# Performance work log

Hardware: AMD Instinct MI355X
Metric: run time of the kernel (lower is better)

Reference implementation:

```python
import jax, jax.numpy as jnp
import numpy as np

N, E, C, O, H, W, K = 32, 512, 64, 128, 64, 64, 3


def setup_inputs() -> dict:
    key = jax.random.key(0)
    k1, k2, k3, k4, k5, k6 = jax.random.split(key, 6)
    scale_w = 1.0 / np.sqrt(E)
    return {
        "embedding": jax.random.normal(k1, (N, E), dtype=jnp.float32),
        "images": jax.random.normal(k2, (N, C, H, W), dtype=jnp.float32),
        "w_weight": jax.random.uniform(k3, (O * C * K * K, E), dtype=jnp.float32, minval=-scale_w, maxval=scale_w),
        "w_bias": jax.random.uniform(k4, (O * C * K * K,), dtype=jnp.float32, minval=-scale_w, maxval=scale_w),
        "b_weight": jax.random.uniform(k5, (O, E), dtype=jnp.float32, minval=-scale_w, maxval=scale_w),
        "b_bias": jax.random.uniform(k6, (O,), dtype=jnp.float32, minval=-scale_w, maxval=scale_w),
    }


def reference(embedding, images, w_weight, w_bias, b_weight, b_bias):
    n, c, h, w = images.shape
    o = b_bias.shape[0]
    # per-sample generated filters and biases
    c1_w = embedding @ w_weight.T + w_bias          # [N, O*C*K*K]
    c1_b = embedding @ b_weight.T + b_bias          # [N, O]
    filt = c1_w.reshape(n, o, c, K, K)              # matches torch view(O, C*K*K)
    # im2col equivalent: pad then gather 3x3 shifted views -> [N,C,K,K,H,W]
    xp = jnp.pad(images, ((0, 0), (0, 0), (1, 1), (1, 1)))
    patches = jnp.stack(
        [xp[:, :, i:i + h, j:j + w] for i in range(K) for j in range(K)], axis=2
    ).reshape(n, c, K, K, h, w)
    out = jnp.einsum('nocij,ncijhw->nohw', filt, patches)
    return out + c1_b[:, :, None, None]
```

## Files before the change

### kernel.cpp

```cpp
#include <hip/hip_runtime.h>
#include <hip/hip_bf16.h>

#define N_  32
#define E_  512
#define C_  64
#define O_  128
#define H_  64
#define W_  64
#define CK9 576
#define M_  (O_*CK9)
#define IMGP_ROWB 9216

typedef __bf16 bf16x8 __attribute__((ext_vector_type(8)));
typedef __bf16 bf16x4 __attribute__((ext_vector_type(4)));
typedef float  f32x4  __attribute__((ext_vector_type(4)));

__device__ __forceinline__ void gload_lds16(const void* g, void* l) {
    typedef __attribute__((address_space(1))) const void gvoid;
    typedef __attribute__((address_space(3))) void lvoid;
    __builtin_amdgcn_global_load_lds((gvoid*)g, (lvoid*)l, 16, 0, 0);
}

__global__ __launch_bounds__(256) void img_pack(
    const float* __restrict__ img, __bf16* __restrict__ imgp)
{
    __shared__ __align__(16) __bf16 ldsT[64 * 72];

    int tid = threadIdx.x;
    int blk = blockIdx.x;
    int n = blk / 66, hh = blk - n * 66;
    char* dst = (char*)imgp + ((size_t)n * 66 + hh) * IMGP_ROWB;

    bf16x8 zero = {(__bf16)0.f, (__bf16)0.f, (__bf16)0.f, (__bf16)0.f,
                   (__bf16)0.f, (__bf16)0.f, (__bf16)0.f, (__bf16)0.f};

    if (hh == 0 || hh == 65) {
#pragma unroll
        for (int j = 0; j < 3; j++) {
            int u = j * 256 + tid;
            if (u < 576) *reinterpret_cast<bf16x8*>(dst + u * 16) = zero;
        }
        return;
    }

    int h = hh - 1;
    const float* srcn = img + (size_t)n * (C_ * H_ * W_) + h * 64;
#pragma unroll
    for (int i = 0; i < 4; i++) {
        int idx = i * 256 + tid;
        int c = idx >> 4, wq = (idx & 15) * 4;
        f32x4 v = *reinterpret_cast<const f32x4*>(srcn + (size_t)c * 4096 + wq);
#pragma unroll
        for (int j = 0; j < 4; j++)
            ldsT[(wq + j) * 72 + c] = (__bf16)v[j];
    }
    __syncthreads();

#pragma unroll
    for (int j = 0; j < 3; j++) {
        int u = j * 256 + tid;
        if (u < 576) {
            int col = u >> 3, s = u & 7;
            bf16x8 val = zero;
            if (col >= 1 && col <= 64) {
                int b = s ^ (col & 7);
                val = *reinterpret_cast<const bf16x8*>(&ldsT[(col - 1) * 72 + b * 8]);
            }
            *reinterpret_cast<bf16x8*>(dst + u * 16) = val;
        }
    }
}

__global__ __launch_bounds__(256) void gen_filters(
    const float* __restrict__ emb, const float* __restrict__ w_weight,
    const float* __restrict__ w_bias, __bf16* __restrict__ filt)
{
    __shared__ __align__(16) __bf16 embS[32 * 520];
    __shared__ __align__(16) __bf16 wS[128 * 40];

    int tid  = threadIdx.x;
    int wave = tid >> 6, lane = tid & 63;
    int quad = lane >> 4, l16 = lane & 15;
    int m0 = blockIdx.x * 128;

#pragma unroll
    for (int i = 0; i < 16; i++) {
        int idx = (i * 256 + tid) * 4;
        int n = idx >> 9, e = idx & 511;
        f32x4 v = *reinterpret_cast<const f32x4*>(emb + n * 512 + e);
        bf16x4 b;
        b[0] = (__bf16)v[0]; b[1] = (__bf16)v[1]; b[2] = (__bf16)v[2]; b[3] = (__bf16)v[3];
        *reinterpret_cast<bf16x4*>(&embS[n * 520 + e]) = b;
    }

    f32x4 acc[2][2];
#pragma unroll
    for (int mi = 0; mi < 2; mi++)
#pragma unroll
        for (int ni = 0; ni < 2; ni++)
            acc[mi][ni] = (f32x4){0.f, 0.f, 0.f, 0.f};

    int sub = tid & 7, rbase = tid >> 3;

    for (int kk = 0; kk < 16; kk++) {
        int k0 = kk * 32;
        __syncthreads();
#pragma unroll
        for (int q = 0; q < 4; q++) {
            int row = rbase + q * 32;
            f32x4 v = *reinterpret_cast<const f32x4*>(
                w_weight + (size_t)(m0 + row) * 512 + k0 + sub * 4);
            bf16x4 b;
            b[0] = (__bf16)v[0]; b[1] = (__bf16)v[1]; b[2] = (__bf16)v[2]; b[3] = (__bf16)v[3];
            *reinterpret_cast<bf16x4*>(&wS[row * 40 + sub * 4]) = b;
        }
        __syncthreads();

        bf16x8 a0 = *reinterpret_cast<const bf16x8*>(&wS[(wave * 32 + l16) * 40 + quad * 8]);
        bf16x8 a1 = *reinterpret_cast<const bf16x8*>(&wS[(wave * 32 + 16 + l16) * 40 + quad * 8]);
        bf16x8 b0 = *reinterpret_cast<const bf16x8*>(&embS[l16 * 520 + k0 + quad * 8]);
        bf16x8 b1 = *reinterpret_cast<const bf16x8*>(&embS[(16 + l16) * 520 + k0 + quad * 8]);
        acc[0][0] = __builtin_amdgcn_mfma_f32_16x16x32_bf16(a0, b0, acc[0][0], 0, 0, 0);
        acc[0][1] = __builtin_amdgcn_mfma_f32_16x16x32_bf16(a0, b1, acc[0][1], 0, 0, 0);
        acc[1][0] = __builtin_amdgcn_mfma_f32_16x16x32_bf16(a1, b0, acc[1][0], 0, 0, 0);
        acc[1][1] = __builtin_amdgcn_mfma_f32_16x16x32_bf16(a1, b1, acc[1][1], 0, 0, 0);
    }

#pragma unroll
    for (int mi = 0; mi < 2; mi++) {
#pragma unroll
        for (int r = 0; r < 4; r++) {
            int m = m0 + wave * 32 + mi * 16 + quad * 4 + r;
            int o = m / 576;
            int rem = m - o * 576;
            int c = rem / 9;
            int t = rem - c * 9;
            int kp = t * 64 + c;
            size_t base = ((size_t)(kp >> 3) << 10) + ((size_t)o << 3) + (kp & 7);
            float bias = w_bias[m];
#pragma unroll
            for (int ni = 0; ni < 2; ni++) {
                int n = ni * 16 + l16;
                filt[(size_t)n * M_ + base] = (__bf16)(acc[mi][ni][r] + bias);
            }
        }
    }
}

__global__ __launch_bounds__(256) void gen_bias(
    const float* __restrict__ emb, const float* __restrict__ b_weight,
    const float* __restrict__ b_bias, float* __restrict__ c1b)
{
    int wid  = (blockIdx.x * 256 + threadIdx.x) >> 6;
    int lane = threadIdx.x & 63;
    int n = wid >> 7, o = wid & 127;
    const float* e = emb + (size_t)n * E_ + lane * 8;
    const float* b = b_weight + (size_t)o * E_ + lane * 8;
    f32x4 e0 = *reinterpret_cast<const f32x4*>(e);
    f32x4 e1 = *reinterpret_cast<const f32x4*>(e + 4);
    f32x4 w0 = *reinterpret_cast<const f32x4*>(b);
    f32x4 w1 = *reinterpret_cast<const f32x4*>(b + 4);
    float s = e0[0]*w0[0] + e0[1]*w0[1] + e0[2]*w0[2] + e0[3]*w0[3]
            + e1[0]*w1[0] + e1[1]*w1[1] + e1[2]*w1[2] + e1[3]*w1[3];
#pragma unroll
    for (int off = 32; off; off >>= 1) s += __shfl_xor(s, off, 64);
    if (lane == 0) c1b[wid] = s + b_bias[o];
}

__global__ __launch_bounds__(256, 2) void conv_gemm(
    const __bf16* __restrict__ imgp, const __bf16* __restrict__ filt,
    const float* __restrict__ c1b, float* __restrict__ out)
{
    __shared__ __align__(16) __bf16 slab[4 * 72 * 64];

    int tid  = threadIdx.x;
    int wave = tid >> 6, lane = tid & 63;
    int quad = lane >> 4, l16 = lane & 15;

    int blk = blockIdx.x;
    int n     = ((blk & 7) << 2) + ((blk >> 3) & 3);
    int strip = blk >> 5;

    const __bf16* fN   = filt + (size_t)n * M_;
    const char*   srcN = (const char*)imgp + (size_t)n * 66 * IMGP_ROWB;
    char*         slabB = (char*)slab;
    int oB = wave * 32 + l16;

    int colA[4][3][2];
#pragma unroll
    for (int cb = 0; cb < 4; cb++)
#pragma unroll
        for (int tj = 0; tj < 3; tj++) {
            int col = cb * 16 + l16 + tj;
#pragma unroll
            for (int ck = 0; ck < 2; ck++)
                colA[cb][tj][ck] = col * 128 + (((quad + ck * 4) ^ (col & 7)) << 4);
        }

    for (int pt2 = 0; pt2 < 2; pt2++) {
        int pt = strip * 2 + pt2;
        int h0 = pt * 2;

        __syncthreads();

        const char* src = srcN + (size_t)h0 * IMGP_ROWB;
#pragma unroll
        for (int j = 0; j < 9; j++)
            gload_lds16(src + (j * 256 + tid) * 16,
                        slabB + (j * 256 + wave * 64) * 16);
        __syncthreads();

        f32x4 acc[2][8];
#pragma unroll
        for (int mi = 0; mi < 2; mi++)
#pragma unroll
            for (int ni = 0; ni < 8; ni++)
                acc[mi][ni] = (f32x4){0.f, 0.f, 0.f, 0.f};

#pragma unroll
        for (int kh = 0; kh < 2; kh++) {
            bf16x8 aR[2][9];
#pragma unroll
            for (int mi = 0; mi < 2; mi++)
#pragma unroll
                for (int t9 = 0; t9 < 9; t9++)
                    aR[mi][t9] = *reinterpret_cast<const bf16x8*>(
                        fN + (((kh * 36 + t9 * 4 + quad) << 10) + ((oB + mi * 16) << 3)));

#pragma unroll
            for (int t9 = 0; t9 < 9; t9++) {
                int kk = kh * 9 + t9;
                int t  = kk >> 1;
                int ck = kk & 1;
                int di = t / 3;
                int tj = t - 3 * di;

                bf16x8 b[8];
#pragma unroll
                for (int ni = 0; ni < 8; ni++) {
                    int row = (ni >> 2) + di;
                    b[ni] = *reinterpret_cast<const bf16x8*>(
                        slabB + row * IMGP_ROWB + colA[ni & 3][tj][ck]);
                }
#pragma unroll
                for (int mi = 0; mi < 2; mi++)
#pragma unroll
                    for (int ni = 0; ni < 8; ni++)
                        acc[mi][ni] = __builtin_amdgcn_mfma_f32_16x16x32_bf16(
                            aR[mi][t9], b[ni], acc[mi][ni], 0, 0, 0);
            }
        }

#pragma unroll
        for (int mi = 0; mi < 2; mi++) {
#pragma unroll
            for (int r = 0; r < 4; r++) {
                int o = wave * 32 + mi * 16 + quad * 4 + r;
                float bias = c1b[(n << 7) + o];
                float* op = out + (((size_t)(n << 7) + o) << 12) + (pt << 7);
#pragma unroll
                for (int ni = 0; ni < 8; ni++)
                    op[(ni >> 2) * 64 + (ni & 3) * 16 + l16] = acc[mi][ni][r] + bias;
            }
        }
    }
}

extern "C" void kernel_launch(void* const* d_in, const int* in_sizes, int n_in,
                              void* d_out, int out_size, void* d_ws, size_t ws_size,
                              hipStream_t stream)
{
    (void)in_sizes; (void)n_in; (void)out_size; (void)ws_size;
    const float* emb      = (const float*)d_in[0];
    const float* images   = (const float*)d_in[1];
    const float* w_weight = (const float*)d_in[2];
    const float* w_bias   = (const float*)d_in[3];
    const float* b_weight = (const float*)d_in[4];
    const float* b_bias   = (const float*)d_in[5];
    float* out = (float*)d_out;

    __bf16* filt = (__bf16*)d_ws;
    float*  c1b  = (float*)((char*)d_ws + (size_t)N_ * M_ * 2);
    __bf16* imgp = (__bf16*)((char*)d_ws + (size_t)N_ * M_ * 2 + 16384);

    img_pack<<<dim3(N_ * 66), dim3(256), 0, stream>>>(images, imgp);
    gen_filters<<<dim3(M_ / 128), dim3(256), 0, stream>>>(emb, w_weight, w_bias, filt);
    gen_bias<<<dim3(N_ * O_ / 4), dim3(256), 0, stream>>>(emb, b_weight, b_bias, c1b);
    conv_gemm<<<dim3(512), dim3(256), 0, stream>>>(imgp, filt, c1b, out);
}
```

Baseline: 333.0 us.

## Merge producer kernels into one launch and restructure conv inner loop and epilogue

Folds img_pack, gen_filters and gen_bias into a single producers kernel that dispatches on block index, which removes two launches and lets the three jobs run concurrently. Filter generation now prefetches the next 64-wide weight chunk into registers, so global loads overlap with the MFMA work. The conv GEMM is reordered to load four slab rows once per (tj, ck) and reuse them across the di offsets. Its epilogue stages results through LDS so output stores are coalesced 16-byte writes, and the bias is hoisted into registers. The costs are higher register pressure, extra LDS barriers in the epilogue, and a larger shared-memory footprint for the fused producer.

```diff
diff --git a/kernel.cpp b/kernel.cpp
--- a/kernel.cpp
+++ b/kernel.cpp
@@ -21,157 +21,168 @@
     __builtin_amdgcn_global_load_lds((gvoid*)g, (lvoid*)l, 16, 0, 0);
 }
 
-__global__ __launch_bounds__(256) void img_pack(
-    const float* __restrict__ img, __bf16* __restrict__ imgp)
+__global__ __launch_bounds__(256, 3) void producers(
+    const float* __restrict__ emb, const float* __restrict__ img,
+    const float* __restrict__ w_weight, const float* __restrict__ w_bias,
+    const float* __restrict__ b_weight, const float* __restrict__ b_bias,
+    __bf16* __restrict__ filt, __bf16* __restrict__ imgp, float* __restrict__ c1b)
 {
-    __shared__ __align__(16) __bf16 ldsT[64 * 72];
-
+    __shared__ __align__(16) char smem[51712];
+    int bid = blockIdx.x;
     int tid = threadIdx.x;
-    int blk = blockIdx.x;
-    int n = blk / 66, hh = blk - n * 66;
-    char* dst = (char*)imgp + ((size_t)n * 66 + hh) * IMGP_ROWB;
-
-    bf16x8 zero = {(__bf16)0.f, (__bf16)0.f, (__bf16)0.f, (__bf16)0.f,
-                   (__bf16)0.f, (__bf16)0.f, (__bf16)0.f, (__bf16)0.f};
-
-    if (hh == 0 || hh == 65) {
+
+    if (bid < 576) {
+        __bf16* embS = (__bf16*)smem;
+        __bf16* wS   = (__bf16*)(smem + 33280);
+
+        int wave = tid >> 6, lane = tid & 63;
+        int quad = lane >> 4, l16 = lane & 15;
+        int m0 = bid * 128;
+
+        int sub = tid & 15, rbase = tid >> 4;
+        const float* wp = w_weight + (size_t)(m0 + rbase) * 512 + sub * 4;
+        f32x4 V[8];
+#pragma unroll
+        for (int q = 0; q < 8; q++)
+            V[q] = *reinterpret_cast<const f32x4*>(wp + q * 16 * 512);
+
+#pragma unroll
+        for (int i = 0; i < 16; i++) {
+            int idx = (i * 256 + tid) * 4;
+            int n = idx >> 9, e = idx & 511;
+            f32x4 v = *reinterpret_cast<const f32x4*>(emb + n * 512 + e);
+            bf16x4 b;
+            b[0] = (__bf16)v[0]; b[1] = (__bf16)v[1]; b[2] = (__bf16)v[2]; b[3] = (__bf16)v[3];
+            *reinterpret_cast<bf16x4*>(&embS[n * 520 + e]) = b;
+        }
+
+        f32x4 acc[2][2];
+#pragma unroll
+        for (int mi = 0; mi < 2; mi++)
+#pragma unroll
+            for (int ni = 0; ni < 2; ni++)
+                acc[mi][ni] = (f32x4){0.f, 0.f, 0.f, 0.f};
+
+        for (int kk = 0; kk < 8; kk++) {
+            int k0 = kk * 64;
+            __syncthreads();
+#pragma unroll
+            for (int q = 0; q < 8; q++) {
+                bf16x4 b;
+                b[0] = (__bf16)V[q][0]; b[1] = (__bf16)V[q][1];
+                b[2] = (__bf16)V[q][2]; b[3] = (__bf16)V[q][3];
+                *reinterpret_cast<bf16x4*>(&wS[(rbase + q * 16) * 72 + sub * 4]) = b;
+            }
+            if (kk < 7) {
+#pragma unroll
+                for (int q = 0; q < 8; q++)
+                    V[q] = *reinterpret_cast<const f32x4*>(wp + q * 16 * 512 + (kk + 1) * 64);
+            }
+            __syncthreads();
+
+#pragma unroll
+            for (int kc = 0; kc < 2; kc++) {
+                bf16x8 a0 = *reinterpret_cast<const bf16x8*>(&wS[(wave * 32 + l16) * 72 + kc * 32 + quad * 8]);
+                bf16x8 a1 = *reinterpret_cast<const bf16x8*>(&wS[(wave * 32 + 16 + l16) * 72 + kc * 32 + quad * 8]);
+                bf16x8 b0 = *reinterpret_cast<const bf16x8*>(&embS[l16 * 520 + k0 + kc * 32 + quad * 8]);
+                bf16x8 b1 = *reinterpret_cast<const bf16x8*>(&embS[(16 + l16) * 520 + k0 + kc * 32 + quad * 8]);
+                acc[0][0] = __builtin_amdgcn_mfma_f32_16x16x32_bf16(a0, b0, acc[0][0], 0, 0, 0);
+                acc[0][1] = __builtin_amdgcn_mfma_f32_16x16x32_bf16(a0, b1, acc[0][1], 0, 0, 0);
+                acc[1][0] = __builtin_amdgcn_mfma_f32_16x16x32_bf16(a1, b0, acc[1][0], 0, 0, 0);
+                acc[1][1] = __builtin_amdgcn_mfma_f32_16x16x32_bf16(a1, b1, acc[1][1], 0, 0, 0);
+            }
+        }
+
+#pragma unroll
+        for (int mi = 0; mi < 2; mi++) {
+#pragma unroll
+            for (int r = 0; r < 4; r++) {
+                int m = m0 + wave * 32 + mi * 16 + quad * 4 + r;
+                int o = m / 576;
+                int rem = m - o * 576;
+                int c = rem / 9;
+                int t = rem - c * 9;
+                int kp = t * 64 + c;
+                size_t base = ((size_t)(kp >> 3) << 10) + ((size_t)o << 3) + (kp & 7);
+                float bias = w_bias[m];
+#pragma unroll
+                for (int ni = 0; ni < 2; ni++) {
+                    int n = ni * 16 + l16;
+                    filt[(size_t)n * M_ + base] = (__bf16)(acc[mi][ni][r] + bias);
+                }
+            }
+        }
+    } else if (bid < 2688) {
+        __bf16* ldsT = (__bf16*)smem;
+        int blk = bid - 576;
+        int n = blk / 66, hh = blk - n * 66;
+        char* dst = (char*)imgp + ((size_t)n * 66 + hh) * IMGP_ROWB;
+
+        bf16x8 zero = {(__bf16)0.f, (__bf16)0.f, (__bf16)0.f, (__bf16)0.f,
+                       (__bf16)0.f, (__bf16)0.f, (__bf16)0.f, (__bf16)0.f};
+
+        if (hh == 0 || hh == 65) {
+#pragma unroll
+            for (int j = 0; j < 3; j++) {
+                int u = j * 256 + tid;
+                if (u < 576) *reinterpret_cast<bf16x8*>(dst + u * 16) = zero;
+            }
+            return;
+        }
+
+        int h = hh - 1;
+        const float* srcn = img + (size_t)n * (C_ * H_ * W_) + h * 64;
+#pragma unroll
+        for (int i = 0; i < 4; i++) {
+            int idx = i * 256 + tid;
+            int c = idx >> 4, wq = (idx & 15) * 4;
+            f32x4 v = *reinterpret_cast<const f32x4*>(srcn + (size_t)c * 4096 + wq);
+#pragma unroll
+            for (int j = 0; j < 4; j++)
+                ldsT[(wq + j) * 72 + c] = (__bf16)v[j];
+        }
+        __syncthreads();
+
 #pragma unroll
         for (int j = 0; j < 3; j++) {
             int u = j * 256 + tid;
-            if (u < 576) *reinterpret_cast<bf16x8*>(dst + u * 16) = zero;
-        }
-        return;
+            if (u < 576) {
+                int col = u >> 3, s = u & 7;
+                bf16x8 val = zero;
+                if (col >= 1 && col <= 64) {
+                    int b = s ^ (col & 7);
+                    val = *reinterpret_cast<const bf16x8*>(&ldsT[(col - 1) * 72 + b * 8]);
+                }
+                *reinterpret_cast<bf16x8*>(dst + u * 16) = val;
+            }
+        }
+    } else {
+        int wave = tid >> 6, lane = tid & 63;
+        int wid = ((bid - 2688) << 2) + wave;
+        int n = wid >> 7, o = wid & 127;
+        const float* e = emb + (size_t)n * E_ + lane * 8;
+        const float* b = b_weight + (size_t)o * E_ + lane * 8;
+        f32x4 e0 = *reinterpret_cast<const f32x4*>(e);
+        f32x4 e1 = *reinterpret_cast<const f32x4*>(e + 4);
+        f32x4 w0 = *reinterpret_cast<const f32x4*>(b);
+        f32x4 w1 = *reinterpret_cast<const f32x4*>(b + 4);
+        float s = e0[0]*w0[0] + e0[1]*w0[1] + e0[2]*w0[2] + e0[3]*w0[3]
+                + e1[0]*w1[0] + e1[1]*w1[1] + e1[2]*w1[2] + e1[3]*w1[3];
+#pragma unroll
+        for (int off = 32; off; off >>= 1) s += __shfl_xor(s, off, 64);
+        if (lane == 0) c1b[wid] = s + b_bias[o];
     }
-
-    int h = hh - 1;
-    const float* srcn = img + (size_t)n * (C_ * H_ * W_) + h * 64;
-#pragma unroll
-    for (int i = 0; i < 4; i++) {
-        int idx = i * 256 + tid;
-        int c = idx >> 4, wq = (idx & 15) * 4;
-        f32x4 v = *reinterpret_cast<const f32x4*>(srcn + (size_t)c * 4096 + wq);
-#pragma unroll
-        for (int j = 0; j < 4; j++)
-            ldsT[(wq + j) * 72 + c] = (__bf16)v[j];
-    }
-    __syncthreads();
-
-#pragma unroll
-    for (int j = 0; j < 3; j++) {
-        int u = j * 256 + tid;
-        if (u < 576) {
-            int col = u >> 3, s = u & 7;
-            bf16x8 val = zero;
-            if (col >= 1 && col <= 64) {
-                int b = s ^ (col & 7);
-                val = *reinterpret_cast<const bf16x8*>(&ldsT[(col - 1) * 72 + b * 8]);
-            }
-            *reinterpret_cast<bf16x8*>(dst + u * 16) = val;
-        }
-    }
-}
-
-__global__ __launch_bounds__(256) void gen_filters(
-    const float* __restrict__ emb, const float* __restrict__ w_weight,
-    const float* __restrict__ w_bias, __bf16* __restrict__ filt)
-{
-    __shared__ __align__(16) __bf16 embS[32 * 520];
-    __shared__ __align__(16) __bf16 wS[128 * 40];
-
-    int tid  = threadIdx.x;
-    int wave = tid >> 6, lane = tid & 63;
-    int quad = lane >> 4, l16 = lane & 15;
-    int m0 = blockIdx.x * 128;
-
-#pragma unroll
-    for (int i = 0; i < 16; i++) {
-        int idx = (i * 256 + tid) * 4;
-        int n = idx >> 9, e = idx & 511;
-        f32x4 v = *reinterpret_cast<const f32x4*>(emb + n * 512 + e);
-        bf16x4 b;
-        b[0] = (__bf16)v[0]; b[1] = (__bf16)v[1]; b[2] = (__bf16)v[2]; b[3] = (__bf16)v[3];
-        *reinterpret_cast<bf16x4*>(&embS[n * 520 + e]) = b;
-    }
-
-    f32x4 acc[2][2];
-#pragma unroll
-    for (int mi = 0; mi < 2; mi++)
-#pragma unroll
-        for (int ni = 0; ni < 2; ni++)
-            acc[mi][ni] = (f32x4){0.f, 0.f, 0.f, 0.f};
-
-    int sub = tid & 7, rbase = tid >> 3;
-
-    for (int kk = 0; kk < 16; kk++) {
-        int k0 = kk * 32;
-        __syncthreads();
-#pragma unroll
-        for (int q = 0; q < 4; q++) {
-            int row = rbase + q * 32;
-            f32x4 v = *reinterpret_cast<const f32x4*>(
-                w_weight + (size_t)(m0 + row) * 512 + k0 + sub * 4);
-            bf16x4 b;
-            b[0] = (__bf16)v[0]; b[1] = (__bf16)v[1]; b[2] = (__bf16)v[2]; b[3] = (__bf16)v[3];
-            *reinterpret_cast<bf16x4*>(&wS[row * 40 + sub * 4]) = b;
-        }
-        __syncthreads();
-
-        bf16x8 a0 = *reinterpret_cast<const bf16x8*>(&wS[(wave * 32 + l16) * 40 + quad * 8]);
-        bf16x8 a1 = *reinterpret_cast<const bf16x8*>(&wS[(wave * 32 + 16 + l16) * 40 + quad * 8]);
-        bf16x8 b0 = *reinterpret_cast<const bf16x8*>(&embS[l16 * 520 + k0 + quad * 8]);
-        bf16x8 b1 = *reinterpret_cast<const bf16x8*>(&embS[(16 + l16) * 520 + k0 + quad * 8]);
-        acc[0][0] = __builtin_amdgcn_mfma_f32_16x16x32_bf16(a0, b0, acc[0][0], 0, 0, 0);
-        acc[0][1] = __builtin_amdgcn_mfma_f32_16x16x32_bf16(a0, b1, acc[0][1], 0, 0, 0);
-        acc[1][0] = __builtin_amdgcn_mfma_f32_16x16x32_bf16(a1, b0, acc[1][0], 0, 0, 0);
-        acc[1][1] = __builtin_amdgcn_mfma_f32_16x16x32_bf16(a1, b1, acc[1][1], 0, 0, 0);
-    }
-
-#pragma unroll
-    for (int mi = 0; mi < 2; mi++) {
-#pragma unroll
-        for (int r = 0; r < 4; r++) {
-            int m = m0 + wave * 32 + mi * 16 + quad * 4 + r;
-            int o = m / 576;
-            int rem = m - o * 576;
-            int c = rem / 9;
-            int t = rem - c * 9;
-            int kp = t * 64 + c;
-            size_t base = ((size_t)(kp >> 3) << 10) + ((size_t)o << 3) + (kp & 7);
-            float bias = w_bias[m];
-#pragma unroll
-            for (int ni = 0; ni < 2; ni++) {
-                int n = ni * 16 + l16;
-                filt[(size_t)n * M_ + base] = (__bf16)(acc[mi][ni][r] + bias);
-            }
-        }
-    }
-}
-
-__global__ __launch_bounds__(256) void gen_bias(
-    const float* __restrict__ emb, const float* __restrict__ b_weight,
-    const float* __restrict__ b_bias, float* __restrict__ c1b)
-{
-    int wid  = (blockIdx.x * 256 + threadIdx.x) >> 6;
-    int lane = threadIdx.x & 63;
-    int n = wid >> 7, o = wid & 127;
-    const float* e = emb + (size_t)n * E_ + lane * 8;
-    const float* b = b_weight + (size_t)o * E_ + lane * 8;
-    f32x4 e0 = *reinterpret_cast<const f32x4*>(e);
-    f32x4 e1 = *reinterpret_cast<const f32x4*>(e + 4);
-    f32x4 w0 = *reinterpret_cast<const f32x4*>(b);
-    f32x4 w1 = *reinterpret_cast<const f32x4*>(b + 4);
-    float s = e0[0]*w0[0] + e0[1]*w0[1] + e0[2]*w0[2] + e0[3]*w0[3]
-            + e1[0]*w1[0] + e1[1]*w1[1] + e1[2]*w1[2] + e1[3]*w1[3];
-#pragma unroll
-    for (int off = 32; off; off >>= 1) s += __shfl_xor(s, off, 64);
-    if (lane == 0) c1b[wid] = s + b_bias[o];
 }
 
 __global__ __launch_bounds__(256, 2) void conv_gemm(
     const __bf16* __restrict__ imgp, const __bf16* __restrict__ filt,
     const float* __restrict__ c1b, float* __restrict__ out)
 {
-    __shared__ __align__(16) __bf16 slab[4 * 72 * 64];
+    __shared__ __align__(16) char smemc[36864];
+    __bf16* slab  = (__bf16*)smemc;
+    float*  ep    = (float*)smemc;
+    char*   slabB = smemc;
+    (void)slab;
 
     int tid  = threadIdx.x;
     int wave = tid >> 6, lane = tid & 63;
@@ -183,8 +194,14 @@
 
     const __bf16* fN   = filt + (size_t)n * M_;
     const char*   srcN = (const char*)imgp + (size_t)n * 66 * IMGP_ROWB;
-    char*         slabB = (char*)slab;
     int oB = wave * 32 + l16;
+
+    float biasv[2][4];
+#pragma unroll
+    for (int mi = 0; mi < 2; mi++)
+#pragma unroll
+        for (int r = 0; r < 4; r++)
+            biasv[mi][r] = c1b[(n << 7) + wave * 32 + mi * 16 + quad * 4 + r];
 
     int colA[4][3][2];
 #pragma unroll
@@ -218,49 +235,59 @@
                 acc[mi][ni] = (f32x4){0.f, 0.f, 0.f, 0.f};
 
 #pragma unroll
-        for (int kh = 0; kh < 2; kh++) {
-            bf16x8 aR[2][9];
-#pragma unroll
-            for (int mi = 0; mi < 2; mi++)
-#pragma unroll
-                for (int t9 = 0; t9 < 9; t9++)
-                    aR[mi][t9] = *reinterpret_cast<const bf16x8*>(
-                        fN + (((kh * 36 + t9 * 4 + quad) << 10) + ((oB + mi * 16) << 3)));
-
-#pragma unroll
-            for (int t9 = 0; t9 < 9; t9++) {
-                int kk = kh * 9 + t9;
-                int t  = kk >> 1;
-                int ck = kk & 1;
-                int di = t / 3;
-                int tj = t - 3 * di;
-
-                bf16x8 b[8];
-#pragma unroll
-                for (int ni = 0; ni < 8; ni++) {
-                    int row = (ni >> 2) + di;
-                    b[ni] = *reinterpret_cast<const bf16x8*>(
-                        slabB + row * IMGP_ROWB + colA[ni & 3][tj][ck]);
-                }
+        for (int tj = 0; tj < 3; tj++) {
+#pragma unroll
+            for (int ck = 0; ck < 2; ck++) {
+                bf16x8 aR2[2][3];
 #pragma unroll
                 for (int mi = 0; mi < 2; mi++)
 #pragma unroll
-                    for (int ni = 0; ni < 8; ni++)
-                        acc[mi][ni] = __builtin_amdgcn_mfma_f32_16x16x32_bf16(
-                            aR[mi][t9], b[ni], acc[mi][ni], 0, 0, 0);
+                    for (int di = 0; di < 3; di++) {
+                        int kk = 2 * (di * 3 + tj) + ck;
+                        aR2[mi][di] = *reinterpret_cast<const bf16x8*>(
+                            fN + (((kk * 4 + quad) << 10) + ((oB + mi * 16) << 3)));
+                    }
+                bf16x8 b2[4][4];
+#pragma unroll
+                for (int row = 0; row < 4; row++)
+#pragma unroll
+                    for (int cb = 0; cb < 4; cb++)
+                        b2[row][cb] = *reinterpret_cast<const bf16x8*>(
+                            slabB + row * IMGP_ROWB + colA[cb][tj][ck]);
+#pragma unroll
+                for (int di = 0; di < 3; di++)
+#pragma unroll
+                    for (int mi = 0; mi < 2; mi++)
+#pragma unroll
+                        for (int lh = 0; lh < 2; lh++)
+#pragma unroll
+                            for (int cb = 0; cb < 4; cb++)
+                                acc[mi][(lh << 2) | cb] = __builtin_amdgcn_mfma_f32_16x16x32_bf16(
+                                    aR2[mi][di], b2[lh + di][cb], acc[mi][(lh << 2) | cb], 0, 0, 0);
             }
         }
 
 #pragma unroll
         for (int mi = 0; mi < 2; mi++) {
-#pragma unroll
-            for (int r = 0; r < 4; r++) {
-                int o = wave * 32 + mi * 16 + quad * 4 + r;
-                float bias = c1b[(n << 7) + o];
-                float* op = out + (((size_t)(n << 7) + o) << 12) + (pt << 7);
-#pragma unroll
-                for (int ni = 0; ni < 8; ni++)
-                    op[(ni >> 2) * 64 + (ni & 3) * 16 + l16] = acc[mi][ni][r] + bias;
+            __syncthreads();
+#pragma unroll
+            for (int ni = 0; ni < 8; ni++) {
+                int lh = ni >> 2, cb = ni & 3;
+#pragma unroll
+                for (int r = 0; r < 4; r++)
+                    ep[wave * 2112 + (quad * 4 + r) * 132 + lh * 64 + cb * 16 + l16] =
+                        acc[mi][ni][r] + biasv[mi][r];
+            }
+            __syncthreads();
+#pragma unroll
+            for (int u = 0; u < 8; u++) {
+                int idx = u * 256 + tid;
+                int row = idx >> 5, s16 = idx & 31;
+                int w2 = row >> 4, ol = row & 15;
+                f32x4 v = *reinterpret_cast<const f32x4*>(&ep[w2 * 2112 + ol * 132 + s16 * 4]);
+                int o = w2 * 32 + mi * 16 + ol;
+                *reinterpret_cast<f32x4*>(
+                    out + (((size_t)(n << 7) + o) << 12) + (pt << 7) + s16 * 4) = v;
             }
         }
     }
@@ -283,8 +310,7 @@
     float*  c1b  = (float*)((char*)d_ws + (size_t)N_ * M_ * 2);
     __bf16* imgp = (__bf16*)((char*)d_ws + (size_t)N_ * M_ * 2 + 16384);
 
-    img_pack<<<dim3(N_ * 66), dim3(256), 0, stream>>>(images, imgp);
-    gen_filters<<<dim3(M_ / 128), dim3(256), 0, stream>>>(emb, w_weight, w_bias, filt);
-    gen_bias<<<dim3(N_ * O_ / 4), dim3(256), 0, stream>>>(emb, b_weight, b_bias, c1b);
+    producers<<<dim3(3712), dim3(256), 0, stream>>>(
+        emb, images, w_weight, w_bias, b_weight, b_bias, filt, imgp, c1b);
     conv_gemm<<<dim3(512), dim3(256), 0, stream>>>(imgp, filt, c1b, out);
 }
```

Measured after the change: 306.0 us. 8.1% less time.
